# Kernel tuning notes

Measured on AMD Instinct MI355X. Metric: run time of the kernel, lower is better.

Reference implementation:

```python
import jax, jax.numpy as jnp
import numpy as np

N = 32768       # tokens
D_IN = 1024     # input_dim
D_OUT = 1024    # output_dim
E = 8           # num_experts
TOP_K = 2


def setup_inputs() -> dict:
    key = jax.random.key(0)
    k1, k2, k3, k4, k5 = jax.random.split(key, 5)
    scale = 1.0 / np.sqrt(D_IN)
    return {
        "x": jax.random.normal(k1, (N, D_IN), dtype=jnp.float32),
        "Wg": jax.random.uniform(k2, (E, D_IN), jnp.float32, -scale, scale),
        "bg": jax.random.uniform(k3, (E,), jnp.float32, -scale, scale),
        "W": jax.random.uniform(k4, (E, D_OUT, D_IN), jnp.float32, -scale, scale),
        "b": jax.random.uniform(k5, (E, D_OUT), jnp.float32, -scale, scale),
    }


def reference(x, Wg, bg, W, b):
    # Gating: softmax over experts, then top-k (weights NOT renormalized,
    # matching the original module).
    gate_scores = x @ Wg.T + bg                      # [N, E]
    gate_probs = jax.nn.softmax(gate_scores, axis=-1)
    topk_w, topk_idx = jax.lax.top_k(gate_probs, TOP_K)  # [N, K]

    # Per-token combine weight for each expert: sum_k w_k * onehot(idx_k)
    combine = (jax.nn.one_hot(topk_idx, E, dtype=x.dtype)
               * topk_w[..., None]).sum(axis=1)      # [N, E]

    # Dense per-expert GEMM + weighted combine (loop over small fixed E).
    out = jnp.zeros((x.shape[0], D_OUT), dtype=x.dtype)
    for e in range(E):
        out = out + combine[:, e:e + 1] * (x @ W[e].T + b[e])
    return out
```

## Files before the change

kernel.cpp:

```cpp
#include <hip/hip_runtime.h>
#include <hip/hip_bf16.h>
#include <cstdint>
#include <cstddef>

#define N_TOK   32768
#define D_IN    1024
#define D_OUT   1024
#define NE      8

#define BM 128
#define BN 128
#define BK 64
#define NKT (D_IN / BK)

typedef __attribute__((ext_vector_type(4))) float floatx4;
typedef __attribute__((ext_vector_type(8))) short bf16x8;

__device__ __forceinline__ unsigned short f2bf(float f) {
  union { float f; unsigned int u; } v; v.f = f;
  unsigned int u = v.u + 0x7fffu + ((v.u >> 16) & 1u);
  return (unsigned short)(u >> 16);
}

__device__ __forceinline__ unsigned short f2h(float f) {
  union { _Float16 hf; unsigned short us; } c; c.hf = (_Float16)f; return c.us;
}
__device__ __forceinline__ float h2f(unsigned short u) {
  union { _Float16 hf; unsigned short us; } c; c.us = u; return (float)c.hf;
}

__device__ __forceinline__ void gload_lds16(const void* g, void* l) {
  __builtin_amdgcn_global_load_lds(
      (const __attribute__((address_space(1))) unsigned int*)g,
      (__attribute__((address_space(3))) unsigned int*)l, 16, 0, 0);
}

__global__ __launch_bounds__(256) void prep_kernel(
    const float* __restrict__ x,
    const float* __restrict__ Wg,
    const float* __restrict__ bg,
    const float* __restrict__ W,
    unsigned short* __restrict__ xb,
    unsigned short* __restrict__ Wb,
    int* __restrict__ counts,
    int* __restrict__ bids,
    float* __restrict__ bw,
    int* __restrict__ tok2slot,
    float* __restrict__ out,
    int zero_out)
{
  __shared__ float wg_lds[NE * D_IN];
  __shared__ int lcnt[NE];
  __shared__ int basee[NE];
  __shared__ int   tok_e[64][2];
  __shared__ int   tok_s[64][2];
  __shared__ float tok_w[64][2];

  const int blk = blockIdx.x;
  const int tid = threadIdx.x;

  if (blk >= 1024) {
    if (!zero_out) return;
    float4* o4 = (float4*)out;
    const int base = (blk - 1024) * 4096;
#pragma unroll
    for (int i = 0; i < 16; ++i)
      o4[base + i * 256 + tid] = (float4){0.f, 0.f, 0.f, 0.f};
    return;
  }
  if (blk >= 512) {
    const float4* s = (const float4*)W;
    const int base = (blk - 512) * 4096;
#pragma unroll
    for (int i = 0; i < 16; ++i) {
      int idx = base + i * 256 + tid;
      float4 v = s[idx];
      ushort4 h;
      h.x = f2bf(v.x); h.y = f2bf(v.y); h.z = f2bf(v.z); h.w = f2bf(v.w);
      ((ushort4*)Wb)[idx] = h;
    }
    return;
  }

  {
    const float4* s = (const float4*)Wg;
    float4* d = (float4*)wg_lds;
    for (int i = tid; i < NE * D_IN / 4; i += 256) d[i] = s[i];
  }
  if (tid < NE) lcnt[tid] = 0;
  __syncthreads();

  const int wave = tid >> 6, lane = tid & 63;
  const float4* x4 = (const float4*)x;
  const float4* w4 = (const float4*)wg_lds;

  for (int t = 0; t < 16; ++t) {
    const int lt = wave * 16 + t;
    const int n  = blk * 64 + lt;
    float4 xv[4];
    float acc[NE];
#pragma unroll
    for (int e = 0; e < NE; ++e) acc[e] = 0.f;
#pragma unroll
    for (int j = 0; j < 4; ++j) {
      xv[j] = x4[(size_t)n * 256 + j * 64 + lane];
#pragma unroll
      for (int e = 0; e < NE; ++e) {
        float4 w = w4[e * 256 + j * 64 + lane];
        acc[e] += xv[j].x * w.x + xv[j].y * w.y + xv[j].z * w.z + xv[j].w * w.w;
      }
    }
#pragma unroll
    for (int j = 0; j < 4; ++j) {
      ushort4 h;
      h.x = f2bf(xv[j].x); h.y = f2bf(xv[j].y);
      h.z = f2bf(xv[j].z); h.w = f2bf(xv[j].w);
      ((ushort4*)xb)[(size_t)n * 256 + j * 64 + lane] = h;
    }
#pragma unroll
    for (int e = 0; e < NE; ++e)
#pragma unroll
      for (int s = 32; s > 0; s >>= 1)
        acc[e] += __shfl_xor(acc[e], s, 64);

    if (lane == 0) {
      float sc[NE];
#pragma unroll
      for (int e = 0; e < NE; ++e) sc[e] = acc[e] + bg[e];
      float m = sc[0];
#pragma unroll
      for (int e = 1; e < NE; ++e) m = fmaxf(m, sc[e]);
      float p[NE], den = 0.f;
#pragma unroll
      for (int e = 0; e < NE; ++e) { p[e] = __expf(sc[e] - m); den += p[e]; }
      int e1 = 0;
#pragma unroll
      for (int e = 1; e < NE; ++e) if (sc[e] > sc[e1]) e1 = e;
      int e2 = (e1 == 0) ? 1 : 0;
#pragma unroll
      for (int e = 0; e < NE; ++e) if (e != e1 && sc[e] > sc[e2]) e2 = e;
      float inv = 1.f / den;
      tok_e[lt][0] = e1; tok_w[lt][0] = p[e1] * inv; tok_s[lt][0] = atomicAdd(&lcnt[e1], 1);
      tok_e[lt][1] = e2; tok_w[lt][1] = p[e2] * inv; tok_s[lt][1] = atomicAdd(&lcnt[e2], 1);
    }
  }
  __syncthreads();
  if (tid < NE) basee[tid] = atomicAdd(&counts[tid], lcnt[tid]);
  __syncthreads();
  if (tid < 128) {
    int lt = tid >> 1, kk = tid & 1;
    int e = tok_e[lt][kk];
    int slot = basee[e] + tok_s[lt][kk];
    int token = blk * 64 + lt;
    bids[e * N_TOK + slot] = token;
    bw[e * N_TOK + slot]   = tok_w[lt][kk];
    tok2slot[token * 2 + kk] = (e << 15) | slot;
  }
}

__global__ __launch_bounds__(256, 3) void moe_gemm_kernel(
    const unsigned short* __restrict__ xb,
    const unsigned short* __restrict__ Wb,
    const float* __restrict__ bias,
    const int* __restrict__ counts,
    const int* __restrict__ bids,
    const float* __restrict__ bw,
    float* __restrict__ out,
    void* __restrict__ y,
    int mode)
{
  const int bid = blockIdx.x;
  const int e   = bid & 7;
  const int nt  = (bid >> 3) & 7;
  const int mt  = bid >> 6;
  const int cnt = counts[e];
  const int row0 = mt << 7;
  if (row0 >= cnt) return;
  const int rows = min(BM, cnt - row0);

  __shared__ alignas(16) unsigned short Ald[BM * BK];
  __shared__ alignas(16) unsigned short Bld[BN * BK];
  __shared__ int   ids[BM];
  __shared__ float wts[BM];

  const int tid = threadIdx.x;
  if (tid < BM) {
    int src = (tid < rows) ? tid : 0;
    ids[tid] = bids[e * N_TOK + row0 + src];
    wts[tid] = (tid < rows) ? bw[e * N_TOK + row0 + tid] : 0.f;
  }
  __syncthreads();

  const int w    = tid >> 6;
  const int lane = tid & 63;
  const int wm   = w >> 1, wn = w & 1;
  const int m16  = lane & 15;
  const int quad = lane >> 4;

  const unsigned short* wbe = Wb + (size_t)e * D_OUT * D_IN;

  int a_off[4], b_off[4];
  int lds_off[4];
#pragma unroll
  for (int l = 0; l < 4; ++l) {
    const int q = l * 256 + tid;
    const int r = q >> 3;
    const int c = (q & 7) ^ (r & 7);
    a_off[l] = ids[r] * D_IN + c * 8;
    b_off[l] = (nt * BN + r) * D_IN + c * 8;
    lds_off[l] = (l * 256 + w * 64) * 8;
  }

  floatx4 acc[4][4];
#pragma unroll
  for (int i = 0; i < 4; ++i)
#pragma unroll
    for (int j = 0; j < 4; ++j) acc[i][j] = (floatx4){0.f, 0.f, 0.f, 0.f};

  for (int kt = 0; kt < NKT; ++kt) {
    const int kb = kt * BK;
#pragma unroll
    for (int l = 0; l < 4; ++l)
      gload_lds16(xb + a_off[l] + kb, &Ald[lds_off[l]]);
#pragma unroll
    for (int l = 0; l < 4; ++l)
      gload_lds16(wbe + b_off[l] + kb, &Bld[lds_off[l]]);

    asm volatile("s_waitcnt vmcnt(0)" ::: "memory");
    __builtin_amdgcn_s_barrier();
    asm volatile("" ::: "memory");

#pragma unroll
    for (int ks = 0; ks < 2; ++ks) {
      const int sw = (((ks << 2) | quad) ^ (m16 & 7)) * 8;
      bf16x8 af[4], bf[4];
#pragma unroll
      for (int j = 0; j < 4; ++j)
        bf[j] = *(const bf16x8*)&Bld[(wn * 64 + j * 16 + m16) * BK + sw];
#pragma unroll
      for (int i = 0; i < 4; ++i)
        af[i] = *(const bf16x8*)&Ald[(wm * 64 + i * 16 + m16) * BK + sw];
      __builtin_amdgcn_s_setprio(1);
#pragma unroll
      for (int i = 0; i < 4; ++i)
#pragma unroll
        for (int j = 0; j < 4; ++j)
          acc[i][j] = __builtin_amdgcn_mfma_f32_16x16x32_bf16(af[i], bf[j], acc[i][j], 0, 0, 0);
      __builtin_amdgcn_s_setprio(0);
    }

    asm volatile("" ::: "memory");
    __builtin_amdgcn_s_barrier();
    asm volatile("" ::: "memory");
  }

  float bv[4];
  int col[4];
#pragma unroll
  for (int j = 0; j < 4; ++j) {
    col[j] = nt * BN + wn * 64 + j * 16 + m16;
    bv[j] = bias[e * D_OUT + col[j]];
  }

  int ybase = 0;
  if (mode) {
#pragma unroll
    for (int i = 0; i < NE; ++i) ybase += (i < e) ? counts[i] : 0;
  }

#pragma unroll
  for (int i = 0; i < 4; ++i) {
#pragma unroll
    for (int r = 0; r < 4; ++r) {
      int rl = wm * 64 + i * 16 + quad * 4 + r;
      if (rl < rows) {
        float wgt = wts[rl];
        if (mode == 0) {
          float* orow = out + (size_t)ids[rl] * D_OUT;
#pragma unroll
          for (int j = 0; j < 4; ++j)
            atomicAdd(&orow[col[j]], wgt * (acc[i][j][r] + bv[j]));
        } else if (mode == 2) {
          float* yrow = (float*)y + (size_t)(ybase + row0 + rl) * D_OUT;
#pragma unroll
          for (int j = 0; j < 4; ++j)
            yrow[col[j]] = wgt * (acc[i][j][r] + bv[j]);
        } else {
          unsigned short* yrow = (unsigned short*)y + (size_t)(ybase + row0 + rl) * D_OUT;
#pragma unroll
          for (int j = 0; j < 4; ++j)
            yrow[col[j]] = f2h(wgt * (acc[i][j][r] + bv[j]));
        }
      }
    }
  }
}

__global__ __launch_bounds__(256) void combine_kernel(
    const void* __restrict__ y,
    const int* __restrict__ counts,
    const int* __restrict__ tok2slot,
    float* __restrict__ out,
    int mode)
{
  __shared__ int pre[NE];
  if (threadIdx.x < NE) {
    int s = 0;
    for (int i = 0; i < threadIdx.x; ++i) s += counts[i];
    pre[threadIdx.x] = s;
  }
  __syncthreads();

  const int total = N_TOK * (D_OUT / 4);
  for (int idx = blockIdx.x * 256 + threadIdx.x; idx < total; idx += 2048 * 256) {
    int row = idx >> 8, c4 = idx & 255;
    int v1 = tok2slot[row * 2], v2 = tok2slot[row * 2 + 1];
    long r1 = pre[v1 >> 15] + (v1 & 32767);
    long r2 = pre[v2 >> 15] + (v2 & 32767);
    float4 o;
    if (mode == 2) {
      const float4* y4 = (const float4*)y;
      float4 a = y4[r1 * 256 + c4];
      float4 b = y4[r2 * 256 + c4];
      o.x = a.x + b.x; o.y = a.y + b.y; o.z = a.z + b.z; o.w = a.w + b.w;
    } else {
      const ushort4* y4 = (const ushort4*)y;
      ushort4 a = y4[r1 * 256 + c4];
      ushort4 b = y4[r2 * 256 + c4];
      o.x = h2f(a.x) + h2f(b.x); o.y = h2f(a.y) + h2f(b.y);
      o.z = h2f(a.z) + h2f(b.z); o.w = h2f(a.w) + h2f(b.w);
    }
    ((float4*)out)[idx] = o;
  }
}

extern "C" void kernel_launch(void* const* d_in, const int* in_sizes, int n_in,
                              void* d_out, int out_size, void* d_ws, size_t ws_size,
                              hipStream_t stream) {
  const float* x  = (const float*)d_in[0];
  const float* Wg = (const float*)d_in[1];
  const float* bg = (const float*)d_in[2];
  const float* W  = (const float*)d_in[3];
  const float* b  = (const float*)d_in[4];
  float* out = (float*)d_out;

  char* ws = (char*)d_ws;
  size_t off = 0;
  int*   counts   = (int*)(ws + off);  off += 4096;
  int*   bids     = (int*)(ws + off);  off += (size_t)NE * N_TOK * 4;
  float* bw       = (float*)(ws + off); off += (size_t)NE * N_TOK * 4;
  int*   tok2slot = (int*)(ws + off);  off += (size_t)N_TOK * 2 * 4;
  unsigned short* xb = (unsigned short*)(ws + off); off += (size_t)N_TOK * D_IN * 2;
  unsigned short* Wb = (unsigned short*)(ws + off); off += (size_t)NE * D_IN * D_OUT * 2;
  void* y = (void*)(ws + off);
  const size_t y_rows = 2 * (size_t)N_TOK;
  const size_t need_f32 = off + y_rows * D_OUT * 4;
  const size_t need_f16 = off + y_rows * D_OUT * 2;

  int mode = (ws_size >= need_f32) ? 2 : (ws_size >= need_f16 ? 1 : 0);

  hipMemsetAsync(counts, 0, NE * sizeof(int), stream);
  prep_kernel<<<mode == 0 ? 3072 : 1024, 256, 0, stream>>>(
      x, Wg, bg, W, xb, Wb, counts, bids, bw, tok2slot, out, mode == 0 ? 1 : 0);
  moe_gemm_kernel<<<NE * 8 * (N_TOK / BM), 256, 0, stream>>>(
      xb, Wb, b, counts, bids, bw, out, y, mode);
  if (mode != 0)
    combine_kernel<<<2048, 256, 0, stream>>>(y, counts, tok2slot, out, mode);
}
```

Before: 511.0 us.

## Restructure gating kernel to process four tokens per 16-lane group, raise GEMM occupancy

```diff
diff --git a/kernel.cpp b/kernel.cpp
--- a/kernel.cpp
+++ b/kernel.cpp
@@ -83,67 +83,85 @@
   }
 
   {
-    const float4* s = (const float4*)Wg;
+    const float4* sp = (const float4*)Wg;
     float4* d = (float4*)wg_lds;
-    for (int i = tid; i < NE * D_IN / 4; i += 256) d[i] = s[i];
+    for (int i = tid; i < NE * D_IN / 4; i += 256) d[i] = sp[i];
   }
   if (tid < NE) lcnt[tid] = 0;
   __syncthreads();
 
-  const int wave = tid >> 6, lane = tid & 63;
+  const int w = tid >> 6, lane = tid & 63;
+  const int g = lane >> 4, s = lane & 15;
   const float4* x4 = (const float4*)x;
   const float4* w4 = (const float4*)wg_lds;
 
-  for (int t = 0; t < 16; ++t) {
-    const int lt = wave * 16 + t;
-    const int n  = blk * 64 + lt;
-    float4 xv[4];
-    float acc[NE];
-#pragma unroll
-    for (int e = 0; e < NE; ++e) acc[e] = 0.f;
-#pragma unroll
-    for (int j = 0; j < 4; ++j) {
-      xv[j] = x4[(size_t)n * 256 + j * 64 + lane];
-#pragma unroll
-      for (int e = 0; e < NE; ++e) {
-        float4 w = w4[e * 256 + j * 64 + lane];
-        acc[e] += xv[j].x * w.x + xv[j].y * w.y + xv[j].z * w.z + xv[j].w * w.w;
-      }
-    }
-#pragma unroll
-    for (int j = 0; j < 4; ++j) {
+  int nbase[4];
+#pragma unroll
+  for (int rr = 0; rr < 4; ++rr)
+    nbase[rr] = (blk * 64 + w * 16 + g * 4 + rr) * 256;
+
+  float acc[4][NE];
+#pragma unroll
+  for (int rr = 0; rr < 4; ++rr)
+#pragma unroll
+    for (int e = 0; e < NE; ++e) acc[rr][e] = 0.f;
+
+#pragma unroll
+  for (int j = 0; j < 16; ++j) {
+    float4 wg_e[NE];
+#pragma unroll
+    for (int e = 0; e < NE; ++e) wg_e[e] = w4[e * 256 + j * 16 + s];
+#pragma unroll
+    for (int rr = 0; rr < 4; ++rr) {
+      float4 xv = x4[(size_t)nbase[rr] + j * 16 + s];
       ushort4 h;
-      h.x = f2bf(xv[j].x); h.y = f2bf(xv[j].y);
-      h.z = f2bf(xv[j].z); h.w = f2bf(xv[j].w);
-      ((ushort4*)xb)[(size_t)n * 256 + j * 64 + lane] = h;
-    }
-#pragma unroll
-    for (int e = 0; e < NE; ++e)
-#pragma unroll
-      for (int s = 32; s > 0; s >>= 1)
-        acc[e] += __shfl_xor(acc[e], s, 64);
-
-    if (lane == 0) {
-      float sc[NE];
-#pragma unroll
-      for (int e = 0; e < NE; ++e) sc[e] = acc[e] + bg[e];
-      float m = sc[0];
-#pragma unroll
-      for (int e = 1; e < NE; ++e) m = fmaxf(m, sc[e]);
-      float p[NE], den = 0.f;
-#pragma unroll
-      for (int e = 0; e < NE; ++e) { p[e] = __expf(sc[e] - m); den += p[e]; }
-      int e1 = 0;
-#pragma unroll
-      for (int e = 1; e < NE; ++e) if (sc[e] > sc[e1]) e1 = e;
-      int e2 = (e1 == 0) ? 1 : 0;
-#pragma unroll
-      for (int e = 0; e < NE; ++e) if (e != e1 && sc[e] > sc[e2]) e2 = e;
-      float inv = 1.f / den;
+      h.x = f2bf(xv.x); h.y = f2bf(xv.y); h.z = f2bf(xv.z); h.w = f2bf(xv.w);
+      ((ushort4*)xb)[(size_t)nbase[rr] + j * 16 + s] = h;
+#pragma unroll
+      for (int e = 0; e < NE; ++e)
+        acc[rr][e] += xv.x * wg_e[e].x + xv.y * wg_e[e].y +
+                      xv.z * wg_e[e].z + xv.w * wg_e[e].w;
+    }
+  }
+
+#pragma unroll
+  for (int rr = 0; rr < 4; ++rr)
+#pragma unroll
+    for (int e = 0; e < NE; ++e) {
+#pragma unroll
+      for (int m = 1; m < 16; m <<= 1)
+        acc[rr][e] += __shfl_xor(acc[rr][e], m, 64);
+    }
+
+  float bgv[NE];
+#pragma unroll
+  for (int e = 0; e < NE; ++e) bgv[e] = bg[e];
+
+#pragma unroll
+  for (int rr = 0; rr < 4; ++rr) {
+    float sc[NE];
+#pragma unroll
+    for (int e = 0; e < NE; ++e) sc[e] = acc[rr][e] + bgv[e];
+    float m = sc[0];
+#pragma unroll
+    for (int e = 1; e < NE; ++e) m = fmaxf(m, sc[e]);
+    float p[NE], den = 0.f;
+#pragma unroll
+    for (int e = 0; e < NE; ++e) { p[e] = __expf(sc[e] - m); den += p[e]; }
+    int e1 = 0;
+#pragma unroll
+    for (int e = 1; e < NE; ++e) if (sc[e] > sc[e1]) e1 = e;
+    int e2 = (e1 == 0) ? 1 : 0;
+#pragma unroll
+    for (int e = 0; e < NE; ++e) if (e != e1 && sc[e] > sc[e2]) e2 = e;
+    float inv = 1.f / den;
+    if (s == 0) {
+      const int lt = w * 16 + g * 4 + rr;
       tok_e[lt][0] = e1; tok_w[lt][0] = p[e1] * inv; tok_s[lt][0] = atomicAdd(&lcnt[e1], 1);
       tok_e[lt][1] = e2; tok_w[lt][1] = p[e2] * inv; tok_s[lt][1] = atomicAdd(&lcnt[e2], 1);
     }
   }
+
   __syncthreads();
   if (tid < NE) basee[tid] = atomicAdd(&counts[tid], lcnt[tid]);
   __syncthreads();
@@ -158,7 +176,7 @@
   }
 }
 
-__global__ __launch_bounds__(256, 3) void moe_gemm_kernel(
+__global__ __launch_bounds__(256, 4) void moe_gemm_kernel(
     const unsigned short* __restrict__ xb,
     const unsigned short* __restrict__ Wb,
     const float* __restrict__ bias,
```

After: 553.5 us. 8.3% more time.
